# Kernel tuning notes

Hardware: AMD Instinct MI355X
Metric: run time of the kernel (lower is better)

## Reference

```python
import jax, jax.numpy as jnp
import numpy as np

N_NODES = 100_000
N_EDGES = 1_600_000
N_GRAPHS = 64
EPS = 1e-7  # GENConv message epsilon
D_IN, D_H, D_OUT, OUT_DIM = 128, 192, 128, 10


def _w(k, fan_in, fan_out):
    return jax.random.normal(k, (fan_in, fan_out), jnp.float32) * (1.0 / np.sqrt(fan_in))


def setup_inputs() -> dict:
    key = jax.random.key(0)
    ks = jax.random.split(key, 8)
    return {
        "x": jax.random.normal(ks[0], (N_NODES, D_IN), jnp.float32),
        "W0": _w(ks[1], D_IN, D_H), "b0": jnp.zeros((D_H,), jnp.float32),
        "W1": _w(ks[2], D_H, D_H), "b1": jnp.zeros((D_H,), jnp.float32),
        "W2": _w(ks[3], D_H, D_H), "b2": jnp.zeros((D_H,), jnp.float32),
        "W3": _w(ks[4], D_H, D_OUT), "b3": jnp.zeros((D_OUT,), jnp.float32),
        "Wfc": _w(ks[5], D_OUT, OUT_DIM), "bfc": jnp.zeros((OUT_DIM,), jnp.float32),
        "edge_index": jax.random.randint(ks[6], (2, N_EDGES), 0, N_NODES, jnp.int32),
        "batch": jnp.sort(jax.random.randint(ks[7], (N_NODES,), 0, N_GRAPHS, jnp.int32)),
    }


def _genconv(x, W, b, src, dst):
    # GENConv (num_layers=1, aggr='add'): message = relu(x_j) + eps,
    # scatter-add to dst, residual add, single Linear MLP.
    msg = jax.nn.relu(x[src]) + EPS          # [E, d]
    agg = jax.ops.segment_sum(msg, dst, num_segments=N_NODES)  # [N, d]
    return (x + agg) @ W + b


def reference(x, W0, b0, W1, b1, W2, b2, W3, b3, Wfc, bfc, edge_index, batch):
    src, dst = edge_index[0], edge_index[1]  # source_to_target flow
    for W, b in ((W0, b0), (W1, b1), (W2, b2), (W3, b3)):
        x = _genconv(x, W, b, src, dst)
    # global mean pool over graphs
    sums = jax.ops.segment_sum(x, batch, num_segments=N_GRAPHS)
    counts = jax.ops.segment_sum(jnp.ones((x.shape[0],), x.dtype), batch,
                                 num_segments=N_GRAPHS)
    pooled = sums / jnp.maximum(counts, 1.0)[:, None]  # [G, D_OUT]
    logits = pooled @ Wfc + bfc                        # [G, OUT_DIM]
    return jax.nn.log_softmax(logits, axis=1)
```

## Files before the change

### kernel.cpp

```cpp
#include <hip/hip_runtime.h>
#include <hip/hip_bf16.h>
#include <stdint.h>

constexpr int NN = 100000;
constexpr int NE = 1600000;
constexpr int NG = 64;
constexpr int S  = 192;
constexpr int NB_SCAN = 98;
constexpr int NN8 = 100352;
constexpr unsigned int ZOFF = (unsigned int)NN * 384u;

constexpr int PREP_INDEG_BLK = 1563;
constexpr int PREP_CONVX_BLK = 12500;
constexpr int PREP_CONVW_BLK = 384;
constexpr int PREP_GB_BLK    = 391;
constexpr int PREP_GRID = PREP_INDEG_BLK + PREP_CONVX_BLK + PREP_CONVW_BLK + PREP_GB_BLK;

constexpr int EG_BLOCKS = 391;
constexpr int HROW = 50048;
constexpr int SROW = HROW / 16;
constexpr int HIST_BLOCKS = NG * 16;
constexpr int POOL_BLOCKS = 2000;

typedef __bf16 bf16x8 __attribute__((ext_vector_type(8)));
typedef float  f32x16 __attribute__((ext_vector_type(16)));
typedef float  f32x2  __attribute__((ext_vector_type(2)));

union U16x4 { uint4 u; bf16x8 b; };

__device__ __forceinline__ float bl(unsigned int u) { return __uint_as_float(u << 16); }
__device__ __forceinline__ float bh(unsigned int u) { return __uint_as_float(u & 0xffff0000u); }
__device__ __forceinline__ float b16f(unsigned short u) { return __uint_as_float(((unsigned int)u) << 16); }
__device__ __forceinline__ unsigned int fb(float f) {
    unsigned int u = __float_as_uint(f);
    return (u + 0x7fffu + ((u >> 16) & 1u)) >> 16;
}
__device__ __forceinline__ unsigned int prelu(unsigned int u) {
    unsigned int r;
    asm("v_pk_max_f16 %0, %1, %2" : "=v"(r) : "v"(u), "v"(0u));
    return r;
}
__device__ __forceinline__ unsigned int cnt2bf(unsigned int h) {
    float f0 = (float)(h & 0xffffu);
    float f1 = (float)(h >> 16);
    return (__float_as_uint(f0) >> 16) | (__float_as_uint(f1) & 0xffff0000u);
}

__global__ __launch_bounds__(256) void k_prep(const float* __restrict__ x,
                                              const int* __restrict__ ei,
                                              const int* __restrict__ bat,
                                              const float* __restrict__ W0, const float* __restrict__ W1,
                                              const float* __restrict__ W2,
                                              unsigned short* __restrict__ A_,
                                              int* __restrict__ indeg8, int* __restrict__ slot,
                                              unsigned short* __restrict__ T0, unsigned short* __restrict__ T1,
                                              unsigned short* __restrict__ T2,
                                              int* __restrict__ nstart) {
    const int b = blockIdx.x;
    if (b < PREP_INDEG_BLK) {
        int e4 = (b * 256 + threadIdx.x) * 4;
        if (e4 < NE) {
            int* cp = indeg8 + (b & 7) * NN8;
            int4 d = *(const int4*)(ei + NE + e4);
            int4 sl;
            sl.x = atomicAdd(&cp[d.x], 1);
            sl.y = atomicAdd(&cp[d.y], 1);
            sl.z = atomicAdd(&cp[d.z], 1);
            sl.w = atomicAdd(&cp[d.w], 1);
            *(int4*)(slot + e4) = sl;
        }
    } else if (b < PREP_INDEG_BLK + PREP_CONVX_BLK) {
        int id = (b - PREP_INDEG_BLK) * 256 + threadIdx.x;
        if (id < 96) ((unsigned int*)(A_ + (size_t)NN * S))[id] = 0u;
        int row = id >> 5, c4 = id & 31;
        float4 v = ((const float4*)x)[id];
        uint2 a;
        a.x = fb(v.x) | (fb(v.y) << 16);
        a.y = fb(v.z) | (fb(v.w) << 16);
        *(uint2*)(A_ + row * S + c4 * 4) = a;
    } else if (b < PREP_INDEG_BLK + PREP_CONVX_BLK + PREP_CONVW_BLK) {
        int id = (b - PREP_INDEG_BLK - PREP_CONVX_BLK) * 256 + threadIdx.x;
        const float* W; unsigned short* T; int N, base;
        if      (id < 24576) { W = W0; T = T0; N = 192; base = 0;     }
        else if (id < 61440) { W = W1; T = T1; N = 192; base = 24576; }
        else                 { W = W2; T = T2; N = 192; base = 61440; }
        int lid = id - base;
        int ci = lid >> 3, j = lid & 7;
        int kc = ci / N, n = ci % N;
        T[lid] = (unsigned short)fb(W[(kc * 8 + j) * N + n]);
    } else {
        int n = (b - PREP_INDEG_BLK - PREP_CONVX_BLK - PREP_CONVW_BLK) * 256 + threadIdx.x;
        if (n < NN) {
            int b0 = bat[n];
            int bprev = (n == 0) ? -1 : bat[n - 1];
            for (int g = bprev + 1; g <= b0; g++) nstart[g] = n;
            if (n == NN - 1)
                for (int g = b0 + 1; g < NG; g++) nstart[g] = NN;
        }
    }
}

__global__ __launch_bounds__(1024) void k_scan1(const int* __restrict__ indeg8,
                                                int* __restrict__ indeg,
                                                unsigned short* __restrict__ pxcd,
                                                int* __restrict__ offs,
                                                int* __restrict__ partials,
                                                float* __restrict__ zero_region) {
    __shared__ int s[1024];
    int t = threadIdx.x;
    int gid = blockIdx.x * 1024 + t;
    int v = 0;
    if (gid < NN) {
        int run = 0;
#pragma unroll
        for (int x = 0; x < 8; x++) {
            int c = indeg8[x * NN8 + gid];
            pxcd[x * NN8 + gid] = (unsigned short)run;
            run += c;
        }
        v = run;
        indeg[gid] = run;
    }
    if (blockIdx.x == 0) {
        for (int i = t; i < 12416; i += 1024) zero_region[i] = 0.f;
    }
    s[t] = v;
    __syncthreads();
    for (int d = 1; d < 1024; d <<= 1) {
        int tv = (t >= d) ? s[t - d] : 0;
        __syncthreads();
        s[t] += tv;
        __syncthreads();
    }
    if (gid < NN) offs[gid + 1] = s[t];
    if (t == 1023) partials[blockIdx.x] = s[1023];
}

__device__ __forceinline__ int toff(const int* __restrict__ offs, const int* __restrict__ part, int j) {
    return j ? (offs[j] + part[(j - 1) >> 10]) : 0;
}

__global__ __launch_bounds__(256) void k_fill(const int* __restrict__ ei, const int* __restrict__ offs,
                                              const int* __restrict__ praw,
                                              const int* __restrict__ slot,
                                              const unsigned short* __restrict__ pxcd,
                                              int* __restrict__ csr,
                                              int* __restrict__ part2) {
    __shared__ int s[128];
    __shared__ int spx[128];
    const int t = threadIdx.x;
    int v = 0;
    if (t < 128) {
        v = (t < NB_SCAN) ? praw[t] : 0;
        s[t] = v;
    }
    __syncthreads();
    for (int d = 1; d < 128; d <<= 1) {
        int tv = (t < 128 && t >= d) ? s[t - d] : 0;
        __syncthreads();
        if (t < 128) s[t] += tv;
        __syncthreads();
    }
    if (t < 128) spx[t] = s[t] - v;
    __syncthreads();
    if (blockIdx.x == 0 && t < NB_SCAN) part2[t] = spx[t];

    int e4 = (blockIdx.x * 256 + t) * 4;
    if (e4 >= NE) return;
    const unsigned short* px = pxcd + (size_t)((e4 >> 10) & 7) * NN8;
    int4 sv = *(const int4*)(ei + e4);
    int4 dv = *(const int4*)(ei + NE + e4);
    int4 sl = *(const int4*)(slot + e4);
    csr[(dv.x ? offs[dv.x] + spx[(dv.x - 1) >> 10] : 0) + px[dv.x] + sl.x] = sv.x;
    csr[(dv.y ? offs[dv.y] + spx[(dv.y - 1) >> 10] : 0) + px[dv.y] + sl.y] = sv.y;
    csr[(dv.z ? offs[dv.z] + spx[(dv.z - 1) >> 10] : 0) + px[dv.z] + sl.z] = sv.z;
    csr[(dv.w ? offs[dv.w] + spx[(dv.w - 1) >> 10] : 0) + px[dv.w] + sl.w] = sv.w;
}

__device__ __forceinline__ void hist_block(int hb, const int* __restrict__ csr,
                                           const int* __restrict__ offs,
                                           const int* __restrict__ part,
                                           const int* __restrict__ nstart,
                                           unsigned int* __restrict__ hist,
                                           unsigned int* __restrict__ hlds) {
    const int g = hb >> 4, q = hb & 15;
    const unsigned int q0 = (unsigned int)(q * SROW);
    for (int i = threadIdx.x; i < SROW; i += 256) hlds[i] = 0u;
    __syncthreads();
    const int s0 = toff(offs, part, nstart[g]);
    const int s1 = (g == NG - 1) ? NE : toff(offs, part, nstart[g + 1]);
    for (int p = s0 + threadIdx.x; p < s1; p += 256) {
        int src = csr[p];
        unsigned int h = (unsigned int)src >> 1;
        if (h - q0 < (unsigned int)SROW)
            atomicAdd(&hlds[h - q0], 1u << (16 * (src & 1)));
    }
    __syncthreads();
    unsigned int* hrow = hist + (size_t)g * HROW + q0;
    for (int i = threadIdx.x; i < SROW; i += 256) hrow[i] = hlds[i];
}

__global__ __launch_bounds__(256, 8) void k_agg128(const unsigned short* __restrict__ Ain,
                                                   unsigned short* __restrict__ Yout,
                                                   const int* __restrict__ offs,
                                                   const int* __restrict__ part,
                                                   const int* __restrict__ indeg,
                                                   const int* __restrict__ csr,
                                                   const int* __restrict__ nstart,
                                                   unsigned int* __restrict__ hist,
                                                   int histBlocks) {
    __shared__ unsigned int hlds[SROW];
    if (blockIdx.x < (unsigned)histBlocks) {
        hist_block(blockIdx.x, csr, offs, part, nstart, hist, hlds);
        return;
    }
    const int vb = blockIdx.x - histBlocks;
    const int w = threadIdx.x >> 6, lane = threadIdx.x & 63;
    const int i = __builtin_amdgcn_readfirstlane(vb * 4 + w);
    const int deg   = __builtin_amdgcn_readfirstlane(indeg[i]);
    const int start = __builtin_amdgcn_readfirstlane(toff(offs, part, i));
    const int fo = lane * 4;
    const char* Ab = (const char*)Ain;

    f32x2 A01;
    {
        unsigned int p = *(const unsigned int*)(Ab + (size_t)i * 384 + fo);
        const float ed = 1e-7f * (float)deg;
        A01 = (f32x2){bl(p) + ed, bh(p) + ed};
    }

    const int* ecsr = csr + start;
    for (int e = 0; e < deg; e += 16) {
        unsigned int off[16];
#pragma unroll
        for (int k = 0; k < 16; k++) {
            int v = ecsr[e + k];
            off[k] = (e + k < deg) ? (unsigned int)v * 384u : ZOFF;
        }
        unsigned int q[16];
#pragma unroll
        for (int k = 0; k < 16; k++)
            q[k] = *(const unsigned int*)(Ab + (size_t)off[k] + fo);
#pragma unroll
        for (int k = 0; k < 16; k++) {
            unsigned int r = prelu(q[k]);
            A01 += (f32x2){bl(r), bh(r)};
        }
    }
    *(unsigned int*)(Yout + (size_t)i * S + lane * 2) =
        fb(A01.x) | (fb(A01.y) << 16);
}

__global__ __launch_bounds__(256) void k_histsolo(const int* __restrict__ csr,
                                                  const int* __restrict__ offs,
                                                  const int* __restrict__ part,
                                                  const int* __restrict__ nstart,
                                                  unsigned int* __restrict__ hist) {
    __shared__ unsigned int hlds[SROW];
    hist_block(blockIdx.x, csr, offs, part, nstart, hist, hlds);
}

__global__ __launch_bounds__(256, 8) void k_agg192(const unsigned short* __restrict__ Ain,
                                                   unsigned short* __restrict__ Yout,
                                                   const int* __restrict__ offs,
                                                   const int* __restrict__ part,
                                                   const int* __restrict__ indeg,
                                                   const int* __restrict__ csr) {
    const int w = threadIdx.x >> 6, lane = threadIdx.x & 63;
    const int i = __builtin_amdgcn_readfirstlane(blockIdx.x * 4 + w);
    const bool act = lane < 48;
    const int deg   = __builtin_amdgcn_readfirstlane(indeg[i]);
    const int start = __builtin_amdgcn_readfirstlane(toff(offs, part, i));
    const int fo = (act ? lane : 47) * 8;
    const char* Ab = (const char*)Ain;

    f32x2 A01, A23;
    {
        uint2 p = *(const uint2*)(Ab + (size_t)i * 384 + fo);
        const float ed = 1e-7f * (float)deg;
        A01 = (f32x2){bl(p.x) + ed, bh(p.x) + ed};
        A23 = (f32x2){bl(p.y) + ed, bh(p.y) + ed};
    }

    const int* ecsr = csr + start;
    for (int e = 0; e < deg; e += 16) {
        unsigned int off[16];
#pragma unroll
        for (int k = 0; k < 16; k++) {
            int v = ecsr[e + k];
            off[k] = (e + k < deg) ? (unsigned int)v * 384u : ZOFF;
        }
        uint2 p[16];
#pragma unroll
        for (int k = 0; k < 16; k++)
            p[k] = *(const uint2*)(Ab + (size_t)off[k] + fo);
#pragma unroll
        for (int k = 0; k < 16; k++) {
            unsigned int rx = prelu(p[k].x), ry = prelu(p[k].y);
            A01 += (f32x2){bl(rx), bh(rx)};
            A23 += (f32x2){bl(ry), bh(ry)};
        }
    }
    if (act) {
        uint2 o;
        o.x = fb(A01.x) | (fb(A01.y) << 16);
        o.y = fb(A23.x) | (fb(A23.y) << 16);
        *(uint2*)(Yout + (size_t)i * S + lane * 4) = o;
    }
}

template <int K, int N>
__global__ __launch_bounds__(256) void k_gemm(const unsigned short* __restrict__ Yin,
                                              const unsigned short* __restrict__ WtC,
                                              const float* __restrict__ bias,
                                              unsigned short* __restrict__ Aout) {
    static_assert(K % 16 == 0 && N % 32 == 0, "");
    const int w = threadIdx.x >> 6, lane = threadIdx.x & 63;
    const int rt = blockIdx.x * 4 + w;
    if (rt >= (NN / 32)) return;
    const int hl = lane >> 5, lr = lane & 31;
    const int row0 = rt * 32;
    f32x16 acc[N / 32];
#pragma unroll
    for (int c = 0; c < N / 32; c++)
#pragma unroll
        for (int r = 0; r < 16; r++) acc[c][r] = 0.f;

    const unsigned short* ap = Yin + (row0 + lr) * S + hl * 8;
    const uint4* b4 = (const uint4*)WtC;
#pragma unroll
    for (int ks = 0; ks < K / 16; ks++) {
        U16x4 a;
        a.u = *(const uint4*)(ap + ks * 16);
#pragma unroll
        for (int c = 0; c < N / 32; c++) {
            U16x4 b;
            b.u = b4[(ks * 2 + hl) * N + c * 32 + lr];
            acc[c] = __builtin_amdgcn_mfma_f32_32x32x16_bf16(a.b, b.b, acc[c], 0, 0, 0);
        }
    }
#pragma unroll
    for (int c = 0; c < N / 32; c++) {
        const int col = c * 32 + lr;
        const float bc = bias[col];
#pragma unroll
        for (int r = 0; r < 16; r++) {
            const int row = row0 + (r & 3) + 8 * (r >> 2) + 4 * hl;
            Aout[row * S + col] = (unsigned short)fb(acc[c][r] + bc);
        }
    }
}

__global__ __launch_bounds__(384) void k_egemm(const unsigned short* __restrict__ X3,
                                               const unsigned int* __restrict__ hist,
                                               float* __restrict__ partials,
                                               const int* __restrict__ bat,
                                               const int* __restrict__ indeg,
                                               float* __restrict__ sums, float* __restrict__ cnt,
                                               float* __restrict__ degsum) {
    if (blockIdx.x < POOL_BLOCKS) {
        const int pb = blockIdx.x;
        const int f = threadIdx.x;
        if (f >= 192) return;
        int n0 = pb * 50;
        int n1 = min(n0 + 50, NN);
        int cur = bat[n0];
        float acc = 0.f;
        int run = 0, dacc = 0;
        for (int n = n0; n < n1; n++) {
            int g = bat[n];
            if (g != cur) {
                atomicAdd(&sums[cur * 192 + f], acc);
                if (f == 0) { atomicAdd(&cnt[cur], (float)run); atomicAdd(&degsum[cur], (float)dacc); }
                acc = 0.f; run = 0; dacc = 0; cur = g;
            }
            acc += b16f(X3[(size_t)n * S + f]);
            run++;
            if (f == 0) dacc += indeg[n];
        }
        atomicAdd(&sums[cur * 192 + f], acc);
        if (f == 0) { atomicAdd(&cnt[cur], (float)run); atomicAdd(&degsum[cur], (float)dacc); }
        return;
    }
    const int b = blockIdx.x - POOL_BLOCKS;
    const int wv = threadIdx.x >> 6, lane = threadIdx.x & 63;
    const int j0 = b * 256;
    const int hl = lane >> 5, lr = lane & 31;
    const int feat = wv * 32 + lr;
    f32x16 acc[2];
#pragma unroll
    for (int m = 0; m < 2; m++)
#pragma unroll
        for (int r = 0; r < 16; r++) acc[m][r] = 0.f;

    for (int kk = 0; kk < 16; kk++) {
        const int jh = (j0 >> 1) + kk * 8 + hl * 4;
        U16x4 af[2];
#pragma unroll
        for (int m = 0; m < 2; m++) {
            uint4 h = *(const uint4*)(hist + (size_t)(m * 32 + lr) * HROW + jh);
            af[m].u = (uint4){cnt2bf(h.x), cnt2bf(h.y), cnt2bf(h.z), cnt2bf(h.w)};
        }
        U16x4 bf;
#pragma unroll
        for (int tp = 0; tp < 4; tp++) {
            int je = j0 + kk * 16 + hl * 8 + tp * 2;
            int ja = min(je, NN), jb = min(je + 1, NN);
            unsigned int u0 = X3[(size_t)ja * S + feat];
            unsigned int u1 = X3[(size_t)jb * S + feat];
            ((unsigned int*)&bf.u)[tp] = prelu(u0 | (u1 << 16));
        }
#pragma unroll
        for (int m = 0; m < 2; m++)
            acc[m] = __builtin_amdgcn_mfma_f32_32x32x16_bf16(af[m].b, bf.b, acc[m], 0, 0, 0);
    }
    float* pb = partials + (size_t)b * 12288;
#pragma unroll
    for (int m = 0; m < 2; m++)
#pragma unroll
        for (int r = 0; r < 16; r++) {
            const int g = m * 32 + (r & 3) + 8 * (r >> 2) + 4 * hl;
            pb[g * 192 + feat] = acc[m][r];
        }
}

__global__ __launch_bounds__(192) void k_head(const float* __restrict__ sums,
                                              const float* __restrict__ partials,
                                              const float* __restrict__ cnt, const float* __restrict__ degsum,
                                              const float* __restrict__ W3, const float* __restrict__ b3,
                                              const float* __restrict__ Wfc, const float* __restrict__ bfc,
                                              float* __restrict__ out) {
    __shared__ float py[192];
    __shared__ float tl[128];
    __shared__ float lg[10];
    const int g = blockIdx.x, t = threadIdx.x;
    const float inv = 1.f / fmaxf(cnt[g], 1.f);
    const float ed = 1e-7f * degsum[g];
    const float* pp = partials + g * 192 + t;
    float s0 = 0.f, s1 = 0.f, s2 = 0.f, s3 = 0.f;
    int p = 0;
    for (; p + 4 <= EG_BLOCKS; p += 4) {
        s0 += pp[(size_t)(p + 0) * 12288];
        s1 += pp[(size_t)(p + 1) * 12288];
        s2 += pp[(size_t)(p + 2) * 12288];
        s3 += pp[(size_t)(p + 3) * 12288];
    }
    for (; p < EG_BLOCKS; p++) s0 += pp[(size_t)p * 12288];
    py[t] = (sums[g * 192 + t] + ((s0 + s1) + (s2 + s3)) + ed) * inv;
    __syncthreads();
    if (t < 128) {
        float tf = b3[t];
        for (int k = 0; k < 192; k++) tf += py[k] * W3[k * 128 + t];
        tl[t] = tf;
    }
    __syncthreads();
    if (t < 10) {
        float sf = bfc[t];
        for (int f = 0; f < 128; f++) sf += tl[f] * Wfc[f * 10 + t];
        lg[t] = sf;
    }
    __syncthreads();
    if (t < 10) {
        float m = lg[0];
        for (int k = 1; k < 10; k++) m = fmaxf(m, lg[k]);
        float se = 0.f;
        for (int k = 0; k < 10; k++) se += expf(lg[k] - m);
        out[g * 10 + t] = lg[t] - m - logf(se);
    }
}

constexpr size_t A0_OFF      = 0;
constexpr size_t A1_OFF      = 38400384;
constexpr size_t SLOT_REL    = 0;
constexpr size_t INDEG8_REL  = 6400000;
constexpr size_t PXCD_REL    = 9611264;
constexpr size_t HIST_REL    = 0;
constexpr size_t PARTS_REL   = 12812288;
constexpr size_t CSR_OFF     = 76800768;
constexpr size_t OFFS_OFF    = 83200768;
constexpr size_t INDEG_OFF   = 83600896;
constexpr size_t SUMS_OFF    = 84000896;
constexpr size_t CNT_OFF     = 84050048;
constexpr size_t DEGS_OFF    = 84050304;
constexpr size_t PART_OFF    = 84050560;
constexpr size_t PART2_OFF   = 84051072;
constexpr size_t NSTART_OFF  = 84051584;
constexpr size_t WT0_OFF     = 84051840;
constexpr size_t WT1_OFF     = 84100992;
constexpr size_t WT2_OFF     = 84174720;
constexpr size_t HIST2_OFF   = 84248576;
constexpr size_t WS_NEED_BIG = 97060864;

extern "C" void kernel_launch(void* const* d_in, const int* in_sizes, int n_in,
                              void* d_out, int out_size, void* d_ws, size_t ws_size,
                              hipStream_t stream) {
    const float* x   = (const float*)d_in[0];
    const float* W0  = (const float*)d_in[1];
    const float* b0  = (const float*)d_in[2];
    const float* W1  = (const float*)d_in[3];
    const float* b1  = (const float*)d_in[4];
    const float* W2  = (const float*)d_in[5];
    const float* b2  = (const float*)d_in[6];
    const float* W3  = (const float*)d_in[7];
    const float* b3  = (const float*)d_in[8];
    const float* Wfc = (const float*)d_in[9];
    const float* bfc = (const float*)d_in[10];
    const int*   ei  = (const int*)d_in[11];
    const int*   bat = (const int*)d_in[12];
    float* out = (float*)d_out;

    char* ws = (char*)d_ws;
    unsigned short* A0  = (unsigned short*)(ws + A0_OFF);
    unsigned short* A1  = (unsigned short*)(ws + A1_OFF);
    int* slot            = (int*)(ws + A1_OFF + SLOT_REL);
    int* indeg8          = (int*)(ws + A1_OFF + INDEG8_REL);
    unsigned short* pxcd = (unsigned short*)(ws + A1_OFF + PXCD_REL);
    float* parts         = (float*)(ws + A1_OFF + PARTS_REL);
    int* csr    = (int*)(ws + CSR_OFF);
    int* offs   = (int*)(ws + OFFS_OFF);
    int* indeg  = (int*)(ws + INDEG_OFF);
    int* part   = (int*)(ws + PART_OFF);
    int* part2  = (int*)(ws + PART2_OFF);
    int* nstart = (int*)(ws + NSTART_OFF);
    unsigned short* Wt0 = (unsigned short*)(ws + WT0_OFF);
    unsigned short* Wt1 = (unsigned short*)(ws + WT1_OFF);
    unsigned short* Wt2 = (unsigned short*)(ws + WT2_OFF);
    float* sums   = (float*)(ws + SUMS_OFF);
    float* cnt    = (float*)(ws + CNT_OFF);
    float* degsum = (float*)(ws + DEGS_OFF);

    const bool big = ws_size >= WS_NEED_BIG;
    unsigned int* hist = (unsigned int*)(big ? (ws + HIST2_OFF) : (ws + A1_OFF + HIST_REL));

    hipMemsetAsync(ws + A1_OFF + INDEG8_REL, 0, 3211264, stream);

    k_prep<<<PREP_GRID, 256, 0, stream>>>(x, ei, bat, W0, W1, W2, A0, indeg8, slot,
                                          Wt0, Wt1, Wt2, nstart);

    k_scan1<<<NB_SCAN, 1024, 0, stream>>>(indeg8, indeg, pxcd, offs, part, sums);
    k_fill<<<(NE / 4 + 255) / 256, 256, 0, stream>>>(ei, offs, part, slot, pxcd, csr, part2);

    const int AGG_GRID  = NN / 4;
    const int GEMM_GRID = (NN / 32 + 3) / 4;
    const int hb = big ? HIST_BLOCKS : 0;

    k_agg128<<<AGG_GRID + hb, 256, 0, stream>>>(A0, A1, offs, part2, indeg, csr,
                                                nstart, hist, hb);
    k_gemm<128, 192><<<GEMM_GRID, 256, 0, stream>>>(A1, Wt0, b0, A0);
    k_agg192<<<AGG_GRID, 256, 0, stream>>>(A0, A1, offs, part2, indeg, csr);
    k_gemm<192, 192><<<GEMM_GRID, 256, 0, stream>>>(A1, Wt1, b1, A0);
    k_agg192<<<AGG_GRID, 256, 0, stream>>>(A0, A1, offs, part2, indeg, csr);
    k_gemm<192, 192><<<GEMM_GRID, 256, 0, stream>>>(A1, Wt2, b2, A0);

    if (!big)
        k_histsolo<<<HIST_BLOCKS, 256, 0, stream>>>(csr, offs, part2, nstart, hist);

    k_egemm<<<POOL_BLOCKS + EG_BLOCKS, 384, 0, stream>>>(A0, hist, parts, bat, indeg,
                                                         sums, cnt, degsum);
    k_head<<<NG, 192, 0, stream>>>(sums, parts, cnt, degsum, W3, b3, Wfc, bfc, out);
}
```

Measured before the change: 609.5 us.

## Replace global-atomic CSR slot counting with LDS-partitioned counting and split head reduction

The in-degree and slot assignment moves out of the prep kernel's global atomics on eight replicated counters into a new kernel. Each block handles one of 64 edge groups and one of 8 node slices, counting with LDS atomics and writing 16-bit per-group counts; the scan and fill stages now work over 64 groups instead of 8. Separately, the 391-way partial-sum reduction in the head kernel is split out into a parallel reduction kernel, so the 64-block head only sums 8 partials. The cost is that every edge-group block reads its full edge range eight times, the scan reads 64 count rows per node, and there are two extra launches.

```diff
diff --git a/kernel.cpp b/kernel.cpp
--- a/kernel.cpp
+++ b/kernel.cpp
@@ -7,14 +7,17 @@
 constexpr int NG = 64;
 constexpr int S  = 192;
 constexpr int NB_SCAN = 98;
-constexpr int NN8 = 100352;
 constexpr unsigned int ZOFF = (unsigned int)NN * 384u;
 
-constexpr int PREP_INDEG_BLK = 1563;
 constexpr int PREP_CONVX_BLK = 12500;
 constexpr int PREP_CONVW_BLK = 384;
 constexpr int PREP_GB_BLK    = 391;
-constexpr int PREP_GRID = PREP_INDEG_BLK + PREP_CONVX_BLK + PREP_CONVW_BLK + PREP_GB_BLK;
+constexpr int PREP_GRID = PREP_CONVX_BLK + PREP_CONVW_BLK + PREP_GB_BLK;
+
+constexpr int EGRP = 64;
+constexpr int EPG  = NE / EGRP;
+constexpr int NSL  = 8;
+constexpr int NPS  = NN / NSL;
 
 constexpr int EG_BLOCKS = 391;
 constexpr int HROW = 50048;
@@ -47,30 +50,16 @@
 }
 
 __global__ __launch_bounds__(256) void k_prep(const float* __restrict__ x,
-                                              const int* __restrict__ ei,
                                               const int* __restrict__ bat,
                                               const float* __restrict__ W0, const float* __restrict__ W1,
                                               const float* __restrict__ W2,
                                               unsigned short* __restrict__ A_,
-                                              int* __restrict__ indeg8, int* __restrict__ slot,
                                               unsigned short* __restrict__ T0, unsigned short* __restrict__ T1,
                                               unsigned short* __restrict__ T2,
                                               int* __restrict__ nstart) {
     const int b = blockIdx.x;
-    if (b < PREP_INDEG_BLK) {
-        int e4 = (b * 256 + threadIdx.x) * 4;
-        if (e4 < NE) {
-            int* cp = indeg8 + (b & 7) * NN8;
-            int4 d = *(const int4*)(ei + NE + e4);
-            int4 sl;
-            sl.x = atomicAdd(&cp[d.x], 1);
-            sl.y = atomicAdd(&cp[d.y], 1);
-            sl.z = atomicAdd(&cp[d.z], 1);
-            sl.w = atomicAdd(&cp[d.w], 1);
-            *(int4*)(slot + e4) = sl;
-        }
-    } else if (b < PREP_INDEG_BLK + PREP_CONVX_BLK) {
-        int id = (b - PREP_INDEG_BLK) * 256 + threadIdx.x;
+    if (b < PREP_CONVX_BLK) {
+        int id = b * 256 + threadIdx.x;
         if (id < 96) ((unsigned int*)(A_ + (size_t)NN * S))[id] = 0u;
         int row = id >> 5, c4 = id & 31;
         float4 v = ((const float4*)x)[id];
@@ -78,8 +67,8 @@
         a.x = fb(v.x) | (fb(v.y) << 16);
         a.y = fb(v.z) | (fb(v.w) << 16);
         *(uint2*)(A_ + row * S + c4 * 4) = a;
-    } else if (b < PREP_INDEG_BLK + PREP_CONVX_BLK + PREP_CONVW_BLK) {
-        int id = (b - PREP_INDEG_BLK - PREP_CONVX_BLK) * 256 + threadIdx.x;
+    } else if (b < PREP_CONVX_BLK + PREP_CONVW_BLK) {
+        int id = (b - PREP_CONVX_BLK) * 256 + threadIdx.x;
         const float* W; unsigned short* T; int N, base;
         if      (id < 24576) { W = W0; T = T0; N = 192; base = 0;     }
         else if (id < 61440) { W = W1; T = T1; N = 192; base = 24576; }
@@ -89,7 +78,7 @@
         int kc = ci / N, n = ci % N;
         T[lid] = (unsigned short)fb(W[(kc * 8 + j) * N + n]);
     } else {
-        int n = (b - PREP_INDEG_BLK - PREP_CONVX_BLK - PREP_CONVW_BLK) * 256 + threadIdx.x;
+        int n = (b - PREP_CONVX_BLK - PREP_CONVW_BLK) * 256 + threadIdx.x;
         if (n < NN) {
             int b0 = bat[n];
             int bprev = (n == 0) ? -1 : bat[n - 1];
@@ -100,9 +89,29 @@
     }
 }
 
-__global__ __launch_bounds__(1024) void k_scan1(const int* __restrict__ indeg8,
+__global__ __launch_bounds__(256) void k_slot(const int* __restrict__ ei,
+                                              int* __restrict__ slot,
+                                              unsigned short* __restrict__ cntg) {
+    __shared__ unsigned int cnt[NPS];
+    const int eg = blockIdx.x >> 3, ns = blockIdx.x & 7;
+    const int nbase = ns * NPS;
+    for (int i = threadIdx.x; i < NPS; i += 256) cnt[i] = 0u;
+    __syncthreads();
+    const int e0 = eg * EPG;
+    for (int e = e0 + threadIdx.x; e < e0 + EPG; e += 256) {
+        int dst = ei[NE + e];
+        unsigned int rel = (unsigned int)(dst - nbase);
+        if (rel < (unsigned int)NPS)
+            slot[e] = (int)atomicAdd(&cnt[rel], 1u);
+    }
+    __syncthreads();
+    unsigned short* outp = cntg + (size_t)eg * NN + nbase;
+    for (int i = threadIdx.x; i < NPS; i += 256) outp[i] = (unsigned short)cnt[i];
+}
+
+__global__ __launch_bounds__(1024) void k_scan1(const unsigned short* __restrict__ cntg,
                                                 int* __restrict__ indeg,
-                                                unsigned short* __restrict__ pxcd,
+                                                unsigned short* __restrict__ pxg,
                                                 int* __restrict__ offs,
                                                 int* __restrict__ partials,
                                                 float* __restrict__ zero_region) {
@@ -112,10 +121,9 @@
     int v = 0;
     if (gid < NN) {
         int run = 0;
-#pragma unroll
-        for (int x = 0; x < 8; x++) {
-            int c = indeg8[x * NN8 + gid];
-            pxcd[x * NN8 + gid] = (unsigned short)run;
+        for (int eg = 0; eg < EGRP; eg++) {
+            int c = cntg[(size_t)eg * NN + gid];
+            pxg[(size_t)eg * NN + gid] = (unsigned short)run;
             run += c;
         }
         v = run;
@@ -143,7 +151,7 @@
 __global__ __launch_bounds__(256) void k_fill(const int* __restrict__ ei, const int* __restrict__ offs,
                                               const int* __restrict__ praw,
                                               const int* __restrict__ slot,
-                                              const unsigned short* __restrict__ pxcd,
+                                              const unsigned short* __restrict__ pxg,
                                               int* __restrict__ csr,
                                               int* __restrict__ part2) {
     __shared__ int s[128];
@@ -167,7 +175,7 @@
 
     int e4 = (blockIdx.x * 256 + t) * 4;
     if (e4 >= NE) return;
-    const unsigned short* px = pxcd + (size_t)((e4 >> 10) & 7) * NN8;
+    const unsigned short* px = pxg + (size_t)(e4 / EPG) * NN;
     int4 sv = *(const int4*)(ei + e4);
     int4 dv = *(const int4*)(ei + NE + e4);
     int4 sl = *(const int4*)(slot + e4);
@@ -424,8 +432,27 @@
         }
 }
 
+__global__ __launch_bounds__(256) void k_reduce(const float* __restrict__ partials,
+                                                float* __restrict__ parts2) {
+    const int j = blockIdx.x / 48;
+    const int gf = (blockIdx.x % 48) * 256 + threadIdx.x;
+    const int p0 = j * 49;
+    const int p1 = min(p0 + 49, EG_BLOCKS);
+    const float* pp = partials + gf;
+    float s0 = 0.f, s1 = 0.f, s2 = 0.f, s3 = 0.f;
+    int p = p0;
+    for (; p + 4 <= p1; p += 4) {
+        s0 += pp[(size_t)(p + 0) * 12288];
+        s1 += pp[(size_t)(p + 1) * 12288];
+        s2 += pp[(size_t)(p + 2) * 12288];
+        s3 += pp[(size_t)(p + 3) * 12288];
+    }
+    for (; p < p1; p++) s0 += pp[(size_t)p * 12288];
+    parts2[(size_t)j * 12288 + gf] = (s0 + s1) + (s2 + s3);
+}
+
 __global__ __launch_bounds__(192) void k_head(const float* __restrict__ sums,
-                                              const float* __restrict__ partials,
+                                              const float* __restrict__ parts2,
                                               const float* __restrict__ cnt, const float* __restrict__ degsum,
                                               const float* __restrict__ W3, const float* __restrict__ b3,
                                               const float* __restrict__ Wfc, const float* __restrict__ bfc,
@@ -436,17 +463,11 @@
     const int g = blockIdx.x, t = threadIdx.x;
     const float inv = 1.f / fmaxf(cnt[g], 1.f);
     const float ed = 1e-7f * degsum[g];
-    const float* pp = partials + g * 192 + t;
-    float s0 = 0.f, s1 = 0.f, s2 = 0.f, s3 = 0.f;
-    int p = 0;
-    for (; p + 4 <= EG_BLOCKS; p += 4) {
-        s0 += pp[(size_t)(p + 0) * 12288];
-        s1 += pp[(size_t)(p + 1) * 12288];
-        s2 += pp[(size_t)(p + 2) * 12288];
-        s3 += pp[(size_t)(p + 3) * 12288];
-    }
-    for (; p < EG_BLOCKS; p++) s0 += pp[(size_t)p * 12288];
-    py[t] = (sums[g * 192 + t] + ((s0 + s1) + (s2 + s3)) + ed) * inv;
+    const float* pp = parts2 + g * 192 + t;
+    float s = 0.f;
+#pragma unroll
+    for (int j = 0; j < 8; j++) s += pp[(size_t)j * 12288];
+    py[t] = (sums[g * 192 + t] + s + ed) * inv;
     __syncthreads();
     if (t < 128) {
         float tf = b3[t];
@@ -472,10 +493,11 @@
 constexpr size_t A0_OFF      = 0;
 constexpr size_t A1_OFF      = 38400384;
 constexpr size_t SLOT_REL    = 0;
-constexpr size_t INDEG8_REL  = 6400000;
-constexpr size_t PXCD_REL    = 9611264;
+constexpr size_t CNTG_REL    = 6400000;
+constexpr size_t PXG_REL     = 19200000;
 constexpr size_t HIST_REL    = 0;
 constexpr size_t PARTS_REL   = 12812288;
+constexpr size_t PARTS2_REL  = 32030720;
 constexpr size_t CSR_OFF     = 76800768;
 constexpr size_t OFFS_OFF    = 83200768;
 constexpr size_t INDEG_OFF   = 83600896;
@@ -513,9 +535,10 @@
     unsigned short* A0  = (unsigned short*)(ws + A0_OFF);
     unsigned short* A1  = (unsigned short*)(ws + A1_OFF);
     int* slot            = (int*)(ws + A1_OFF + SLOT_REL);
-    int* indeg8          = (int*)(ws + A1_OFF + INDEG8_REL);
-    unsigned short* pxcd = (unsigned short*)(ws + A1_OFF + PXCD_REL);
+    unsigned short* cntg = (unsigned short*)(ws + A1_OFF + CNTG_REL);
+    unsigned short* pxg  = (unsigned short*)(ws + A1_OFF + PXG_REL);
     float* parts         = (float*)(ws + A1_OFF + PARTS_REL);
+    float* parts2        = (float*)(ws + A1_OFF + PARTS2_REL);
     int* csr    = (int*)(ws + CSR_OFF);
     int* offs   = (int*)(ws + OFFS_OFF);
     int* indeg  = (int*)(ws + INDEG_OFF);
@@ -532,13 +555,12 @@
     const bool big = ws_size >= WS_NEED_BIG;
     unsigned int* hist = (unsigned int*)(big ? (ws + HIST2_OFF) : (ws + A1_OFF + HIST_REL));
 
-    hipMemsetAsync(ws + A1_OFF + INDEG8_REL, 0, 3211264, stream);
-
-    k_prep<<<PREP_GRID, 256, 0, stream>>>(x, ei, bat, W0, W1, W2, A0, indeg8, slot,
-                                          Wt0, Wt1, Wt2, nstart);
-
-    k_scan1<<<NB_SCAN, 1024, 0, stream>>>(indeg8, indeg, pxcd, offs, part, sums);
-    k_fill<<<(NE / 4 + 255) / 256, 256, 0, stream>>>(ei, offs, part, slot, pxcd, csr, part2);
+
+    k_prep<<<PREP_GRID, 256, 0, stream>>>(x, bat, W0, W1, W2, A0, Wt0, Wt1, Wt2, nstart);
+
+    k_slot<<<EGRP * NSL, 256, 0, stream>>>(ei, slot, cntg);
+    k_scan1<<<NB_SCAN, 1024, 0, stream>>>(cntg, indeg, pxg, offs, part, sums);
+    k_fill<<<(NE / 4 + 255) / 256, 256, 0, stream>>>(ei, offs, part, slot, pxg, csr, part2);
 
     const int AGG_GRID  = NN / 4;
     const int GEMM_GRID = (NN / 32 + 3) / 4;
@@ -557,5 +579,6 @@
 
     k_egemm<<<POOL_BLOCKS + EG_BLOCKS, 384, 0, stream>>>(A0, hist, parts, bat, indeg,
                                                          sums, cnt, degsum);
-    k_head<<<NG, 192, 0, stream>>>(sums, parts, cnt, degsum, W3, b3, Wfc, bfc, out);
-}
+    k_reduce<<<384, 256, 0, stream>>>(parts, parts2);
+    k_head<<<NG, 192, 0, stream>>>(sums, parts2, cnt, degsum, W3, b3, Wfc, bfc, out);
+}
```

Result: slower. 625.2 us (+2.6%).
